# Performance work log

Hardware: AMD Instinct MI355X
Metric: run time of the kernel (lower is better)

The kernel has to match this reference:

```python
import jax, jax.numpy as jnp
import numpy as np

K = 16  # neighbors, incl. self


def setup_inputs() -> dict:
    key = jax.random.key(0)
    ks = jax.random.split(key, 16)
    N, C = 8192, 256  # points, channels (inter_channels == in_channels == C)
    s = 0.05
    inp = {
        'coords': jax.random.uniform(ks[0], (N, 3), dtype=jnp.float32) * 100.0,
        'feats': jax.random.normal(ks[1], (N, C), dtype=jnp.float32),
        'theta_w': jax.random.normal(ks[2], (C, C), dtype=jnp.float32) * s,
        'theta_b': jax.random.normal(ks[3], (C,), dtype=jnp.float32) * s,
        'phi_w': jax.random.normal(ks[4], (C, C), dtype=jnp.float32) * s,
        'phi_b': jax.random.normal(ks[5], (C,), dtype=jnp.float32) * s,
        'g_w': jax.random.normal(ks[6], (C, C), dtype=jnp.float32) * s,
        'g_b': jax.random.normal(ks[7], (C,), dtype=jnp.float32) * s,
        'pe1_w1': jax.random.normal(ks[8], (3, C), dtype=jnp.float32) * s,
        'pe1_b1': jax.random.normal(ks[9], (C,), dtype=jnp.float32) * s,
        'pe1_w2': jax.random.normal(ks[10], (C, C), dtype=jnp.float32) * s,
        'pe1_b2': jax.random.normal(ks[11], (C,), dtype=jnp.float32) * s,
        'W_w': jax.random.normal(ks[12], (C, C), dtype=jnp.float32) * s,
        'W_b': jax.random.normal(ks[13], (C,), dtype=jnp.float32) * s,
    }
    return inp


def reference(coords, feats, theta_w, theta_b, phi_w, phi_b, g_w, g_b,
              pe1_w1, pe1_b1, pe1_w2, pe1_b2, W_w, W_b):
    C = feats.shape[-1]
    # KNN (squared dists, includes self as nearest) == pytorch3d knn_points
    sq = jnp.sum(coords * coords, axis=-1)  # [N]
    d2 = sq[:, None] + sq[None, :] - 2.0 * (coords @ coords.T)  # [N,N]
    _, idx = jax.lax.top_k(-d2, K)  # [N,K] sorted by ascending distance

    nn_coords = coords[idx]            # [N,K,3] knn gather
    nn_feats = feats[idx]              # [N,K,C]

    theta_f = feats @ theta_w + theta_b          # [N,C]
    phi_f = nn_feats @ phi_w + phi_b             # [N,K,C]

    delta_coords = nn_coords - coords[:, None, :]  # [N,K,3]
    # pe1 MLP; NOTE: original code uses pe1 for both pe1 and pe2 (shared)
    pe = jax.nn.relu(delta_coords @ pe1_w1 + pe1_b1) @ pe1_w2 + pe1_b2  # [N,K,C]

    delta_features = (pe * (theta_f[:, None, :] - phi_f) + pe) / jnp.sqrt(jnp.float32(C))
    sim = jax.nn.softmax(delta_features, axis=1)  # softmax over K neighbors

    g_feats = nn_feats @ g_w + g_b               # [N,K,C]
    y = jnp.sum(sim * g_feats, axis=1)           # [N,C]

    # W (1x1 Minkowski conv == per-point linear) + residual
    return y @ W_w + W_b + feats
```

## Files before the change

kernel.cpp:

```cpp
#include <hip/hip_runtime.h>

typedef __bf16 bf16_t;
typedef bf16_t bf16x8 __attribute__((ext_vector_type(8)));
typedef bf16_t bf16x4 __attribute__((ext_vector_type(4)));
typedef bf16_t bf16x2 __attribute__((ext_vector_type(2)));
typedef float f32x4 __attribute__((ext_vector_type(4)));
typedef unsigned long long u64;

#define N_PTS 8192
#define C_DIM 256
#define K_NN 16

#define GRID_G    16
#define GRID_NC   (GRID_G * GRID_G * GRID_G)
#define GRID_CELL 6.25f
#define GRID_INV  0.16f

__global__ __launch_bounds__(256) void cast_feats_kernel(const float* __restrict__ f,
                                                         bf16_t* __restrict__ fb) {
    int i = (blockIdx.x * 256 + threadIdx.x) * 4;
    float4 v = *(const float4*)(f + i);
    bf16x4 o;
    o[0] = (bf16_t)v.x; o[1] = (bf16_t)v.y; o[2] = (bf16_t)v.z; o[3] = (bf16_t)v.w;
    *(bf16x4*)(fb + i) = o;
}

__global__ __launch_bounds__(256) void prep_weights_kernel(
    const float* __restrict__ w0, const float* __restrict__ w1,
    const float* __restrict__ w2, const float* __restrict__ w3,
    const float* __restrict__ w4, bf16_t* __restrict__ wt_base) {
    int m = blockIdx.y;
    const float* src = (m == 0) ? w0 : (m == 1) ? w1 : (m == 2) ? w2 : (m == 3) ? w3 : w4;
    bf16_t* dst = wt_base + m * (C_DIM * C_DIM);
#pragma unroll
    for (int i = 0; i < 4; ++i) {
        int o = blockIdx.x * 1024 + i * 256 + threadIdx.x;
        int tkb = o >> 9;
        int rem = o & 511;
        int lm = rem >> 5;
        int r = rem & 31;
        int k = (tkb & 7) * 32 + r;
        int n = (tkb >> 3) * 16 + lm;
        dst[o] = (bf16_t)src[k * C_DIM + n];
    }
}

__global__ __launch_bounds__(256) void grid_zero_kernel(int* __restrict__ cellCount,
                                                        int* __restrict__ gcount) {
    int i = blockIdx.x * 256 + threadIdx.x;
    cellCount[i] = 0;
    if (i == 0) *gcount = 0;
}

__global__ __launch_bounds__(256) void grid_count_kernel(const float* __restrict__ coords,
                                                         int* __restrict__ cellCount,
                                                         int* __restrict__ cid) {
    int i = blockIdx.x * 256 + threadIdx.x;
    float x = coords[3 * i + 0], y = coords[3 * i + 1], z = coords[3 * i + 2];
    int cx = (int)(x * GRID_INV); if (cx > GRID_G - 1) cx = GRID_G - 1;
    int cy = (int)(y * GRID_INV); if (cy > GRID_G - 1) cy = GRID_G - 1;
    int cz = (int)(z * GRID_INV); if (cz > GRID_G - 1) cz = GRID_G - 1;
    int c = (cx * GRID_G + cy) * GRID_G + cz;
    cid[i] = c;
    atomicAdd(&cellCount[c], 1);
}

__global__ __launch_bounds__(256) void grid_scan_kernel(const int* __restrict__ cellCount,
                                                        int* __restrict__ cellStart,
                                                        int* __restrict__ cellPtr) {
    __shared__ int part[256];
    int t = threadIdx.x;
    int base = t * 16;
    int v[16];
    int sum = 0;
#pragma unroll
    for (int i = 0; i < 16; ++i) { v[i] = cellCount[base + i]; sum += v[i]; }
    part[t] = sum;
    __syncthreads();
    for (int off = 1; off < 256; off <<= 1) {
        int x = (t >= off) ? part[t - off] : 0;
        __syncthreads();
        part[t] += x;
        __syncthreads();
    }
    int acc = part[t] - sum;
#pragma unroll
    for (int i = 0; i < 16; ++i) {
        cellStart[base + i] = acc;
        cellPtr[base + i] = acc;
        acc += v[i];
    }
    if (t == 255) cellStart[GRID_NC] = acc;
}

__global__ __launch_bounds__(256) void grid_scatter_kernel(
    const float* __restrict__ coords, const int* __restrict__ cid, int* __restrict__ cellPtr,
    float* __restrict__ sx, float* __restrict__ sy, float* __restrict__ sz,
    float* __restrict__ ssq, int* __restrict__ sidx) {
    int i = blockIdx.x * 256 + threadIdx.x;
    int c = cid[i];
    int pos = atomicAdd(&cellPtr[c], 1);
    float x = coords[3 * i + 0], y = coords[3 * i + 1], z = coords[3 * i + 2];
    sx[pos] = x; sy[pos] = y; sz[pos] = z;
    ssq[pos] = __fadd_rn(__fadd_rn(__fmul_rn(x, x), __fmul_rn(y, y)), __fmul_rn(z, z));
    sidx[pos] = i;
}

__global__ __launch_bounds__(256) void knn_grid_kernel(
    const float* __restrict__ coords, const int* __restrict__ cellStart,
    const float* __restrict__ sx, const float* __restrict__ sy,
    const float* __restrict__ sz, const float* __restrict__ ssq,
    const int* __restrict__ sidx,
    int* __restrict__ idx_out, int* __restrict__ glist, int* __restrict__ gcount) {
    const int tid = threadIdx.x;
    const int wave = tid >> 6, lane = tid & 63;
    const int q = blockIdx.x * 4 + wave;

    __shared__ int segBase[4][25];
    __shared__ int segPref[4][26];
    __shared__ u64 cand[4][256];
    __shared__ int cnt[4];

    if (lane == 0) cnt[wave] = 0;

    const float qx = coords[3 * q + 0], qy = coords[3 * q + 1], qz = coords[3 * q + 2];
    const float sqi = __fadd_rn(__fadd_rn(__fmul_rn(qx, qx), __fmul_rn(qy, qy)),
                                __fmul_rn(qz, qz));

    int cx = (int)(qx * GRID_INV); if (cx > GRID_G - 1) cx = GRID_G - 1;
    int cy = (int)(qy * GRID_INV); if (cy > GRID_G - 1) cy = GRID_G - 1;
    int cz = (int)(qz * GRID_INV); if (cz > GRID_G - 1) cz = GRID_G - 1;
    int wx0 = cx - 2; if (wx0 < 0) wx0 = 0;
    int wx1 = cx + 2; if (wx1 > GRID_G - 1) wx1 = GRID_G - 1;
    int wy0 = cy - 2; if (wy0 < 0) wy0 = 0;
    int wy1 = cy + 2; if (wy1 > GRID_G - 1) wy1 = GRID_G - 1;
    int wz0 = cz - 2; if (wz0 < 0) wz0 = 0;
    int wz1 = cz + 2; if (wz1 > GRID_G - 1) wz1 = GRID_G - 1;

    const float INF = __int_as_float(0x7f800000);
    float rc = INF;
    if (wx0 > 0)          rc = fminf(rc, qx - (float)wx0 * GRID_CELL);
    if (wx1 < GRID_G - 1) rc = fminf(rc, (float)(wx1 + 1) * GRID_CELL - qx);
    if (wy0 > 0)          rc = fminf(rc, qy - (float)wy0 * GRID_CELL);
    if (wy1 < GRID_G - 1) rc = fminf(rc, (float)(wy1 + 1) * GRID_CELL - qy);
    if (wz0 > 0)          rc = fminf(rc, qz - (float)wz0 * GRID_CELL);
    if (wz1 < GRID_G - 1) rc = fminf(rc, (float)(wz1 + 1) * GRID_CELL - qz);
    float rc2 = rc * rc * 0.9999f;

    int nx = wx1 - wx0 + 1, nyc = wy1 - wy0 + 1;
    int ns = nx * nyc;
    if (lane < ns) {
        int scx = wx0 + lane / nyc;
        int scy = wy0 + lane % nyc;
        int b = (scx * GRID_G + scy) * GRID_G;
        int s0 = cellStart[b + wz0];
        int s1 = cellStart[b + wz1 + 1];
        segBase[wave][lane] = s0;
        segPref[wave][lane] = s1 - s0;
    }
    __syncthreads();
    if (lane == 0) {
        int acc = 0;
        for (int s = 0; s < ns; ++s) { int l = segPref[wave][s]; segPref[wave][s] = acc; acc += l; }
        segPref[wave][ns] = acc;
    }
    __syncthreads();

    const int M = segPref[wave][ns];
    bool flag = (M < K_NN);

    float lmin = INF;
    {
        int s = 0;
        for (int t = lane; t < M; t += 64) {
            while (t >= segPref[wave][s + 1]) ++s;
            int pos = segBase[wave][s] + (t - segPref[wave][s]);
            float x = sx[pos], y = sy[pos], z = sz[pos], sj = ssq[pos];
            float dot = __fmaf_rn(z, qz, __fmaf_rn(y, qy, __fmul_rn(x, qx)));
            float d2 = __fsub_rn(__fadd_rn(sqi, sj), __fmul_rn(2.0f, dot));
            lmin = fminf(lmin, d2);
        }
    }
    float g = fminf(lmin, __shfl_xor(lmin, 1));
    g = fminf(g, __shfl_xor(g, 2));
    float tau = fmaxf(g, __shfl_xor(g, 4));
    tau = fmaxf(tau, __shfl_xor(tau, 8));
    tau = fmaxf(tau, __shfl_xor(tau, 16));
    tau = fmaxf(tau, __shfl_xor(tau, 32));

    {
        int s = 0;
        for (int t = lane; t < M; t += 64) {
            while (t >= segPref[wave][s + 1]) ++s;
            int pos = segBase[wave][s] + (t - segPref[wave][s]);
            float x = sx[pos], y = sy[pos], z = sz[pos], sj = ssq[pos];
            float dot = __fmaf_rn(z, qz, __fmaf_rn(y, qy, __fmul_rn(x, qx)));
            float d2 = __fsub_rn(__fadd_rn(sqi, sj), __fmul_rn(2.0f, dot));
            if (d2 <= tau) {
                unsigned u = __float_as_uint(d2);
                u = (u & 0x80000000u) ? ~u : (u | 0x80000000u);
                int slot = atomicAdd(&cnt[wave], 1);
                if (slot < 256)
                    cand[wave][slot] = (((u64)u) << 32) | (unsigned)sidx[pos];
            }
        }
    }
    __syncthreads();

    int m = cnt[wave];
    if (m > 256) { flag = true; m = 256; }
    u64 k0 = ~0ull, k1 = ~0ull, k2 = ~0ull, k3 = ~0ull;
    if (lane < m) k0 = cand[wave][lane];
    if (lane + 64 < m) k1 = cand[wave][lane + 64];
    if (lane + 128 < m) k2 = cand[wave][lane + 128];
    if (lane + 192 < m) k3 = cand[wave][lane + 192];
    u64 lm2 = k0; int li = 0;
    if (k1 < lm2) { lm2 = k1; li = 1; }
    if (k2 < lm2) { lm2 = k2; li = 2; }
    if (k3 < lm2) { lm2 = k3; li = 3; }
    int keep = 0;
    u64 last = ~0ull;
#pragma unroll 1
    for (int r = 0; r < 16; ++r) {
        u64 w = lm2;
#pragma unroll
        for (int off = 1; off < 64; off <<= 1) {
            u64 o = __shfl_xor(w, off);
            w = (o < w) ? o : w;
        }
        if (lane == r) keep = (int)(unsigned)(w & 0xffffffffull);
        last = w;
        if (lm2 == w) {
            if (li == 0) k0 = ~0ull;
            else if (li == 1) k1 = ~0ull;
            else if (li == 2) k2 = ~0ull;
            else k3 = ~0ull;
            lm2 = k0; li = 0;
            if (k1 < lm2) { lm2 = k1; li = 1; }
            if (k2 < lm2) { lm2 = k2; li = 2; }
            if (k3 < lm2) { lm2 = k3; li = 3; }
        }
    }

    if (!flag) {
        unsigned ou = (unsigned)(last >> 32);
        unsigned db = (ou & 0x80000000u) ? (ou ^ 0x80000000u) : ~ou;
        float d16 = __uint_as_float(db);
        if (d16 >= rc2) flag = true;
    }
    if (flag && lane == 0) {
        int sl = atomicAdd(gcount, 1);
        glist[sl] = q;
    }
    if (lane < 16) idx_out[q * K_NN + lane] = keep;
}

__global__ __launch_bounds__(256) void knn_fallback_kernel(const float* __restrict__ coords,
                                                           const int* __restrict__ glist,
                                                           const int* __restrict__ gcount,
                                                           int* __restrict__ idx_out) {
    const int count = *gcount;
    const int n0 = blockIdx.x * 4;
    if (n0 >= count) return;

    const int tid = threadIdx.x;
    const int wave = tid >> 6, lane = tid & 63;
    __shared__ float red16[4][16];
    __shared__ u64 cand[4][256];
    __shared__ int cnt[4];
    __shared__ int qids[4];

    if (tid < 4) {
        cnt[tid] = 0;
        int slot = n0 + tid;
        qids[tid] = glist[slot < count ? slot : count - 1];
    }
    __syncthreads();

    float qx[4], qy[4], qz[4], sqi[4];
#pragma unroll
    for (int q = 0; q < 4; ++q) {
        int id = qids[q];
        qx[q] = coords[3 * id + 0];
        qy[q] = coords[3 * id + 1];
        qz[q] = coords[3 * id + 2];
        sqi[q] = __fadd_rn(__fadd_rn(__fmul_rn(qx[q], qx[q]), __fmul_rn(qy[q], qy[q])),
                           __fmul_rn(qz[q], qz[q]));
    }

    const float INF = __int_as_float(0x7f800000);
    const float* cp = coords + tid * 96;

    float lmin[4] = {INF, INF, INF, INF};
#pragma unroll
    for (int c = 0; c < 4; ++c) {
        float buf[24];
#pragma unroll
        for (int v = 0; v < 6; ++v)
            *(float4*)(buf + v * 4) = *(const float4*)(cp + c * 24 + v * 4);
#pragma unroll
        for (int p = 0; p < 8; ++p) {
            float x = buf[3 * p + 0], y = buf[3 * p + 1], z = buf[3 * p + 2];
            float sqj = __fadd_rn(__fadd_rn(__fmul_rn(x, x), __fmul_rn(y, y)),
                                  __fmul_rn(z, z));
#pragma unroll
            for (int q = 0; q < 4; ++q) {
                float dot = __fmaf_rn(z, qz[q], __fmaf_rn(y, qy[q], __fmul_rn(x, qx[q])));
                float d2 = __fsub_rn(__fadd_rn(sqi[q], sqj), __fmul_rn(2.0f, dot));
                lmin[q] = fminf(lmin[q], d2);
            }
        }
    }

#pragma unroll
    for (int q = 0; q < 4; ++q) {
        float g = lmin[q];
        g = fminf(g, __shfl_xor(g, 1));
        g = fminf(g, __shfl_xor(g, 2));
        g = fminf(g, __shfl_xor(g, 4));
        g = fminf(g, __shfl_xor(g, 8));
        if ((lane & 15) == 0) red16[q][wave * 4 + (lane >> 4)] = g;
    }
    __syncthreads();

    float tau[4];
#pragma unroll
    for (int q = 0; q < 4; ++q) {
        float t = red16[q][0];
#pragma unroll
        for (int i = 1; i < 16; ++i) t = fmaxf(t, red16[q][i]);
        tau[q] = t;
    }

#pragma unroll
    for (int c = 0; c < 4; ++c) {
        float buf[24];
#pragma unroll
        for (int v = 0; v < 6; ++v)
            *(float4*)(buf + v * 4) = *(const float4*)(cp + c * 24 + v * 4);
#pragma unroll
        for (int p = 0; p < 8; ++p) {
            float x = buf[3 * p + 0], y = buf[3 * p + 1], z = buf[3 * p + 2];
            float sqj = __fadd_rn(__fadd_rn(__fmul_rn(x, x), __fmul_rn(y, y)),
                                  __fmul_rn(z, z));
            int j = tid * 32 + c * 8 + p;
#pragma unroll
            for (int q = 0; q < 4; ++q) {
                float dot = __fmaf_rn(z, qz[q], __fmaf_rn(y, qy[q], __fmul_rn(x, qx[q])));
                float d2 = __fsub_rn(__fadd_rn(sqi[q], sqj), __fmul_rn(2.0f, dot));
                if (d2 <= tau[q]) {
                    unsigned u = __float_as_uint(d2);
                    u = (u & 0x80000000u) ? ~u : (u | 0x80000000u);
                    int slot = atomicAdd(&cnt[q], 1);
                    if (slot < 256)
                        cand[q][slot] = (((u64)u) << 32) | (unsigned)j;
                }
            }
        }
    }
    __syncthreads();

    int m = cnt[wave]; if (m > 256) m = 256;
    u64 k0 = ~0ull, k1 = ~0ull, k2 = ~0ull, k3 = ~0ull;
    if (lane < m) k0 = cand[wave][lane];
    if (lane + 64 < m) k1 = cand[wave][lane + 64];
    if (lane + 128 < m) k2 = cand[wave][lane + 128];
    if (lane + 192 < m) k3 = cand[wave][lane + 192];
    u64 lm2 = k0; int li = 0;
    if (k1 < lm2) { lm2 = k1; li = 1; }
    if (k2 < lm2) { lm2 = k2; li = 2; }
    if (k3 < lm2) { lm2 = k3; li = 3; }
    int keep = 0;
#pragma unroll 1
    for (int r = 0; r < 16; ++r) {
        u64 w = lm2;
#pragma unroll
        for (int off = 1; off < 64; off <<= 1) {
            u64 o = __shfl_xor(w, off);
            w = (o < w) ? o : w;
        }
        if (lane == r) keep = (int)(unsigned)(w & 0xffffffffull);
        if (lm2 == w) {
            if (li == 0) k0 = ~0ull;
            else if (li == 1) k1 = ~0ull;
            else if (li == 2) k2 = ~0ull;
            else k3 = ~0ull;
            lm2 = k0; li = 0;
            if (k1 < lm2) { lm2 = k1; li = 1; }
            if (k2 < lm2) { lm2 = k2; li = 2; }
            if (k3 < lm2) { lm2 = k3; li = 3; }
        }
    }
    if (lane < 16) idx_out[qids[wave] * K_NN + lane] = keep;
}

__global__ __launch_bounds__(256, 2) void proj_kernel(
    const bf16_t* __restrict__ fb, const bf16_t* __restrict__ wt_base,
    const float* __restrict__ tb, const float* __restrict__ pb, const float* __restrict__ gb,
    float* __restrict__ T, bf16_t* __restrict__ PG) {
    const int sel = blockIdx.y;
    const bf16_t* Wt = wt_base + sel * (C_DIM * C_DIM);
    const float* bias = (sel == 0) ? tb : (sel == 1) ? pb : gb;
    const int wave = threadIdx.x >> 6, lane = threadIdx.x & 63;
    const int q = lane >> 4, lm = lane & 15;
    const int m0 = blockIdx.x * 64;

    bf16x8 bfr[4][8];
#pragma unroll
    for (int ti = 0; ti < 4; ++ti)
#pragma unroll
        for (int kb = 0; kb < 8; ++kb)
            bfr[ti][kb] = *(const bf16x8*)(Wt + (((wave * 4 + ti) * 8 + kb) << 9) + lm * 32 + q * 8);

    float bv[4];
#pragma unroll
    for (int ti = 0; ti < 4; ++ti) bv[ti] = bias[(wave * 4 + ti) * 16 + lm];

#pragma unroll
    for (int p = 0; p < 4; ++p) {
        const bf16_t* arow = fb + (m0 + p * 16 + lm) * C_DIM + q * 8;
        bf16x8 a[8];
#pragma unroll
        for (int kb = 0; kb < 8; ++kb) a[kb] = *(const bf16x8*)(arow + kb * 32);
        f32x4 acc[4];
#pragma unroll
        for (int ti = 0; ti < 4; ++ti) acc[ti] = (f32x4){0.f, 0.f, 0.f, 0.f};
#pragma unroll
        for (int ti = 0; ti < 4; ++ti)
#pragma unroll
            for (int kb = 0; kb < 8; ++kb)
                acc[ti] = __builtin_amdgcn_mfma_f32_16x16x32_bf16(a[kb], bfr[ti][kb], acc[ti], 0, 0, 0);

#pragma unroll
        for (int ti = 0; ti < 4; ++ti) {
            int c = (wave * 4 + ti) * 16 + lm;
#pragma unroll
            for (int r = 0; r < 4; ++r) {
                float v = acc[ti][r] + bv[ti];
                int off = (m0 + p * 16 + q * 4 + r) * C_DIM + c;
                if (sel == 0) T[off] = v;
                else if (sel == 1) PG[2 * off] = (bf16_t)v;
                else PG[2 * off + 1] = (bf16_t)v;
            }
        }
    }
}

#define HPAD 264
#define P_BLK 4
#define HROWS (P_BLK * 16)
__global__ __launch_bounds__(256, 2) void pe2_fused_kernel(
    const float* __restrict__ coords, const int* __restrict__ idx,
    const float* __restrict__ T, const bf16_t* __restrict__ PG,
    const float* __restrict__ w1, const float* __restrict__ b1, const float* __restrict__ b2,
    const bf16_t* __restrict__ Wt2, bf16_t* __restrict__ yb) {
    __shared__ __align__(16) bf16_t h_lds[HROWS * HPAD];
    __shared__ float dxyz[HROWS][3];
    __shared__ int idxl[HROWS];
    const int tid = threadIdx.x;
    const int p0 = blockIdx.x * P_BLK;
    const int wave = tid >> 6, lane = tid & 63;
    const int q = lane >> 4, lm = lane & 15;

    bf16x8 bfr[4][8];
#pragma unroll
    for (int ti = 0; ti < 4; ++ti)
#pragma unroll
        for (int kb = 0; kb < 8; ++kb)
            bfr[ti][kb] = *(const bf16x8*)(Wt2 + (((wave * 4 + ti) * 8 + kb) << 9) + lm * 32 + q * 8);
    float b2c[4];
#pragma unroll
    for (int ti = 0; ti < 4; ++ti) b2c[ti] = b2[(wave * 4 + ti) * 16 + lm];

    if (tid < HROWS) {
        int n = p0 + (tid >> 4);
        int j = idx[n * K_NN + (tid & 15)];
        idxl[tid] = j;
        dxyz[tid][0] = coords[3 * j + 0] - coords[3 * n + 0];
        dxyz[tid][1] = coords[3 * j + 1] - coords[3 * n + 1];
        dxyz[tid][2] = coords[3 * j + 2] - coords[3 * n + 2];
    }
    __syncthreads();

    {
        int c = tid;
        float wx = w1[c], wy = w1[C_DIM + c], wz = w1[2 * C_DIM + c], bb = b1[c];
#pragma unroll 4
        for (int r = 0; r < HROWS; ++r) {
            float pre = dxyz[r][0] * wx + dxyz[r][1] * wy + dxyz[r][2] * wz + bb;
            h_lds[r * HPAD + c] = (bf16_t)fmaxf(pre, 0.0f);
        }
    }
    __syncthreads();

#pragma unroll 1
    for (int lp = 0; lp < P_BLK; ++lp) {
        const int n = p0 + lp;

        int jr[4];
#pragma unroll
        for (int r = 0; r < 4; ++r) jr[r] = idxl[lp * 16 + q * 4 + r];
        bf16x2 pg[4][4];
        float Tn[4];
#pragma unroll
        for (int ti = 0; ti < 4; ++ti) {
            int c = (wave * 4 + ti) * 16 + lm;
            Tn[ti] = T[n * C_DIM + c];
#pragma unroll
            for (int r = 0; r < 4; ++r)
                pg[ti][r] = *(const bf16x2*)(PG + 2 * (jr[r] * C_DIM + c));
        }

        const bf16_t* hrow = h_lds + (lp * 16 + lm) * HPAD + q * 8;
        bf16x8 a[8];
#pragma unroll
        for (int kb = 0; kb < 8; ++kb) a[kb] = *(const bf16x8*)(hrow + kb * 32);
        f32x4 acc[4];
#pragma unroll
        for (int ti = 0; ti < 4; ++ti) acc[ti] = (f32x4){0.f, 0.f, 0.f, 0.f};
#pragma unroll
        for (int ti = 0; ti < 4; ++ti)
#pragma unroll
            for (int kb = 0; kb < 8; ++kb)
                acc[ti] = __builtin_amdgcn_mfma_f32_16x16x32_bf16(a[kb], bfr[ti][kb], acc[ti], 0, 0, 0);

#pragma unroll
        for (int ti = 0; ti < 4; ++ti) {
            int c = (wave * 4 + ti) * 16 + lm;
            float df[4];
#pragma unroll
            for (int r = 0; r < 4; ++r) {
                float pe = acc[ti][r] + b2c[ti];
                df[r] = (pe * (Tn[ti] - (float)pg[ti][r][0]) + pe) * 0.0625f;
            }
            float mx = fmaxf(fmaxf(df[0], df[1]), fmaxf(df[2], df[3]));
            mx = fmaxf(mx, __shfl_xor(mx, 16));
            mx = fmaxf(mx, __shfl_xor(mx, 32));
            float e[4], s = 0.f;
#pragma unroll
            for (int r = 0; r < 4; ++r) { e[r] = __expf(df[r] - mx); s += e[r]; }
            s += __shfl_xor(s, 16);
            s += __shfl_xor(s, 32);
            float inv = 1.0f / s;
            float y = 0.f;
#pragma unroll
            for (int r = 0; r < 4; ++r) y += e[r] * inv * (float)pg[ti][r][1];
            y += __shfl_xor(y, 16);
            y += __shfl_xor(y, 32);
            if (q == 0) yb[n * C_DIM + c] = (bf16_t)y;
        }
    }
}

__global__ __launch_bounds__(256, 2) void final_kernel(
    const bf16_t* __restrict__ yb, const bf16_t* __restrict__ Wt,
    const float* __restrict__ Wb, const float* __restrict__ feats,
    float* __restrict__ out) {
    const int wave = threadIdx.x >> 6, lane = threadIdx.x & 63;
    const int q = lane >> 4, lm = lane & 15;
    const int m0 = blockIdx.x * 64;

    bf16x8 bfr[4][8];
#pragma unroll
    for (int ti = 0; ti < 4; ++ti)
#pragma unroll
        for (int kb = 0; kb < 8; ++kb)
            bfr[ti][kb] = *(const bf16x8*)(Wt + (((wave * 4 + ti) * 8 + kb) << 9) + lm * 32 + q * 8);
    float bv[4];
#pragma unroll
    for (int ti = 0; ti < 4; ++ti) bv[ti] = Wb[(wave * 4 + ti) * 16 + lm];

#pragma unroll
    for (int p = 0; p < 4; ++p) {
        const bf16_t* arow = yb + (m0 + p * 16 + lm) * C_DIM + q * 8;
        bf16x8 a[8];
#pragma unroll
        for (int kb = 0; kb < 8; ++kb) a[kb] = *(const bf16x8*)(arow + kb * 32);
        f32x4 acc[4];
#pragma unroll
        for (int ti = 0; ti < 4; ++ti) acc[ti] = (f32x4){0.f, 0.f, 0.f, 0.f};
#pragma unroll
        for (int ti = 0; ti < 4; ++ti)
#pragma unroll
            for (int kb = 0; kb < 8; ++kb)
                acc[ti] = __builtin_amdgcn_mfma_f32_16x16x32_bf16(a[kb], bfr[ti][kb], acc[ti], 0, 0, 0);

#pragma unroll
        for (int ti = 0; ti < 4; ++ti) {
            int c = (wave * 4 + ti) * 16 + lm;
#pragma unroll
            for (int r = 0; r < 4; ++r) {
                int off = (m0 + p * 16 + q * 4 + r) * C_DIM + c;
                out[off] = acc[ti][r] + bv[ti] + feats[off];
            }
        }
    }
}

extern "C" void kernel_launch(void* const* d_in, const int* in_sizes, int n_in,
                              void* d_out, int out_size, void* d_ws, size_t ws_size,
                              hipStream_t stream) {
    const float* coords = (const float*)d_in[0];
    const float* feats  = (const float*)d_in[1];
    const float* theta_w = (const float*)d_in[2];
    const float* theta_b = (const float*)d_in[3];
    const float* phi_w   = (const float*)d_in[4];
    const float* phi_b   = (const float*)d_in[5];
    const float* g_w     = (const float*)d_in[6];
    const float* g_b     = (const float*)d_in[7];
    const float* pe1_w1  = (const float*)d_in[8];
    const float* pe1_b1  = (const float*)d_in[9];
    const float* pe1_w2  = (const float*)d_in[10];
    const float* pe1_b2  = (const float*)d_in[11];
    const float* W_w     = (const float*)d_in[12];
    const float* W_b     = (const float*)d_in[13];
    float* out = (float*)d_out;

    char* w = (char*)d_ws;
    size_t off = 0;
    int* idx = (int*)(w + off);        off += (size_t)N_PTS * K_NN * 4;
    bf16_t* fb = (bf16_t*)(w + off);   off += (size_t)N_PTS * C_DIM * 2;
    bf16_t* wt = (bf16_t*)(w + off);   off += (size_t)5 * C_DIM * C_DIM * 2;
    float* T = (float*)(w + off);      off += (size_t)N_PTS * C_DIM * 4;
    bf16_t* PG = (bf16_t*)(w + off);   off += (size_t)N_PTS * C_DIM * 4;
    bf16_t* yb = (bf16_t*)(w + off);   off += (size_t)N_PTS * C_DIM * 2;
    int* cid       = (int*)(w + off);  off += (size_t)N_PTS * 4;
    int* cellCount = (int*)(w + off);  off += (size_t)GRID_NC * 4;
    int* cellStart = (int*)(w + off);  off += (size_t)(GRID_NC + 1) * 4;
    int* cellPtr   = (int*)(w + off);  off += (size_t)GRID_NC * 4;
    float* sxp = (float*)(w + off);    off += (size_t)N_PTS * 4;
    float* syp = (float*)(w + off);    off += (size_t)N_PTS * 4;
    float* szp = (float*)(w + off);    off += (size_t)N_PTS * 4;
    float* ssqp = (float*)(w + off);   off += (size_t)N_PTS * 4;
    int* sidxp = (int*)(w + off);      off += (size_t)N_PTS * 4;
    int* glist = (int*)(w + off);      off += (size_t)N_PTS * 4;
    int* gcount = (int*)(w + off);     off += 256;
    (void)ws_size; (void)in_sizes; (void)n_in; (void)out_size;

    cast_feats_kernel<<<(N_PTS * C_DIM) / 1024, 256, 0, stream>>>(feats, fb);
    prep_weights_kernel<<<dim3(64, 5), 256, 0, stream>>>(theta_w, phi_w, g_w, pe1_w2, W_w, wt);

    grid_zero_kernel<<<GRID_NC / 256, 256, 0, stream>>>(cellCount, gcount);
    grid_count_kernel<<<N_PTS / 256, 256, 0, stream>>>(coords, cellCount, cid);
    grid_scan_kernel<<<1, 256, 0, stream>>>(cellCount, cellStart, cellPtr);
    grid_scatter_kernel<<<N_PTS / 256, 256, 0, stream>>>(coords, cid, cellPtr,
                                                         sxp, syp, szp, ssqp, sidxp);
    knn_grid_kernel<<<N_PTS / 4, 256, 0, stream>>>(coords, cellStart, sxp, syp, szp,
                                                   ssqp, sidxp, idx, glist, gcount);
    knn_fallback_kernel<<<N_PTS / 4, 256, 0, stream>>>(coords, glist, gcount, idx);

    proj_kernel<<<dim3(N_PTS / 64, 3), 256, 0, stream>>>(fb, wt, theta_b, phi_b, g_b, T, PG);
    pe2_fused_kernel<<<N_PTS / P_BLK, 256, 0, stream>>>(coords, idx, T, PG,
                                                        pe1_w1, pe1_b1, pe1_b2,
                                                        wt + 3 * C_DIM * C_DIM, yb);
    final_kernel<<<N_PTS / 64, 256, 0, stream>>>(yb, wt + 4 * C_DIM * C_DIM, W_b, feats, out);
}
```

Before: 226.0 us.

## Fuse grid build, feature cast and weight prep into one kernel; enlarge pe2 block

Merges six small launches (feature cast, weight transpose/cast, grid zero/count/scan/scatter) into a single kernel. Block 0 builds the whole spatial grid using LDS atomics, while the other blocks do the casts concurrently. This removes launch overhead and the global-memory round trips for cell counts. Separately, pe2_fused_kernel now processes 8 points per block instead of 4. That doubles its LDS tile and may reduce occupancy.

```diff
diff --git a/kernel.cpp b/kernel.cpp
--- a/kernel.cpp
+++ b/kernel.cpp
@@ -16,94 +16,97 @@
 #define GRID_CELL 6.25f
 #define GRID_INV  0.16f
 
-__global__ __launch_bounds__(256) void cast_feats_kernel(const float* __restrict__ f,
-                                                         bf16_t* __restrict__ fb) {
-    int i = (blockIdx.x * 256 + threadIdx.x) * 4;
-    float4 v = *(const float4*)(f + i);
-    bf16x4 o;
-    o[0] = (bf16_t)v.x; o[1] = (bf16_t)v.y; o[2] = (bf16_t)v.z; o[3] = (bf16_t)v.w;
-    *(bf16x4*)(fb + i) = o;
-}
-
-__global__ __launch_bounds__(256) void prep_weights_kernel(
+#define CAST_NBLK 2048
+#define PREPW_NBLK 320
+__global__ __launch_bounds__(256) void fused_prep_kernel(
+    const float* __restrict__ feats, bf16_t* __restrict__ fb,
     const float* __restrict__ w0, const float* __restrict__ w1,
     const float* __restrict__ w2, const float* __restrict__ w3,
-    const float* __restrict__ w4, bf16_t* __restrict__ wt_base) {
-    int m = blockIdx.y;
-    const float* src = (m == 0) ? w0 : (m == 1) ? w1 : (m == 2) ? w2 : (m == 3) ? w3 : w4;
-    bf16_t* dst = wt_base + m * (C_DIM * C_DIM);
-#pragma unroll
-    for (int i = 0; i < 4; ++i) {
-        int o = blockIdx.x * 1024 + i * 256 + threadIdx.x;
-        int tkb = o >> 9;
-        int rem = o & 511;
-        int lm = rem >> 5;
-        int r = rem & 31;
-        int k = (tkb & 7) * 32 + r;
-        int n = (tkb >> 3) * 16 + lm;
-        dst[o] = (bf16_t)src[k * C_DIM + n];
-    }
-}
-
-__global__ __launch_bounds__(256) void grid_zero_kernel(int* __restrict__ cellCount,
-                                                        int* __restrict__ gcount) {
-    int i = blockIdx.x * 256 + threadIdx.x;
-    cellCount[i] = 0;
-    if (i == 0) *gcount = 0;
-}
-
-__global__ __launch_bounds__(256) void grid_count_kernel(const float* __restrict__ coords,
-                                                         int* __restrict__ cellCount,
-                                                         int* __restrict__ cid) {
-    int i = blockIdx.x * 256 + threadIdx.x;
-    float x = coords[3 * i + 0], y = coords[3 * i + 1], z = coords[3 * i + 2];
-    int cx = (int)(x * GRID_INV); if (cx > GRID_G - 1) cx = GRID_G - 1;
-    int cy = (int)(y * GRID_INV); if (cy > GRID_G - 1) cy = GRID_G - 1;
-    int cz = (int)(z * GRID_INV); if (cz > GRID_G - 1) cz = GRID_G - 1;
-    int c = (cx * GRID_G + cy) * GRID_G + cz;
-    cid[i] = c;
-    atomicAdd(&cellCount[c], 1);
-}
-
-__global__ __launch_bounds__(256) void grid_scan_kernel(const int* __restrict__ cellCount,
-                                                        int* __restrict__ cellStart,
-                                                        int* __restrict__ cellPtr) {
-    __shared__ int part[256];
-    int t = threadIdx.x;
-    int base = t * 16;
-    int v[16];
-    int sum = 0;
-#pragma unroll
-    for (int i = 0; i < 16; ++i) { v[i] = cellCount[base + i]; sum += v[i]; }
-    part[t] = sum;
-    __syncthreads();
-    for (int off = 1; off < 256; off <<= 1) {
-        int x = (t >= off) ? part[t - off] : 0;
+    const float* __restrict__ w4, bf16_t* __restrict__ wt_base,
+    const float* __restrict__ coords, int* __restrict__ cellStart,
+    float* __restrict__ sx, float* __restrict__ sy, float* __restrict__ sz,
+    float* __restrict__ ssq, int* __restrict__ sidx, int* __restrict__ gcount) {
+    const int b = blockIdx.x;
+    const int t = threadIdx.x;
+
+    if (b == 0) {
+        __shared__ int cCnt[GRID_NC];
+        __shared__ int part[256];
+        for (int i = t; i < GRID_NC; i += 256) cCnt[i] = 0;
+        if (t == 0) *gcount = 0;
         __syncthreads();
-        part[t] += x;
+
+        int ci[32];
+#pragma unroll
+        for (int k = 0; k < 32; ++k) {
+            int i = t + k * 256;
+            float x = coords[3 * i + 0], y = coords[3 * i + 1], z = coords[3 * i + 2];
+            int cx = (int)(x * GRID_INV); if (cx > GRID_G - 1) cx = GRID_G - 1;
+            int cy = (int)(y * GRID_INV); if (cy > GRID_G - 1) cy = GRID_G - 1;
+            int cz = (int)(z * GRID_INV); if (cz > GRID_G - 1) cz = GRID_G - 1;
+            int c = (cx * GRID_G + cy) * GRID_G + cz;
+            ci[k] = c;
+            atomicAdd(&cCnt[c], 1);
+        }
         __syncthreads();
-    }
-    int acc = part[t] - sum;
-#pragma unroll
-    for (int i = 0; i < 16; ++i) {
-        cellStart[base + i] = acc;
-        cellPtr[base + i] = acc;
-        acc += v[i];
-    }
-    if (t == 255) cellStart[GRID_NC] = acc;
-}
-
-__global__ __launch_bounds__(256) void grid_scatter_kernel(
-    const float* __restrict__ coords, const int* __restrict__ cid, int* __restrict__ cellPtr,
-    float* __restrict__ sx, float* __restrict__ sy, float* __restrict__ sz,
-    float* __restrict__ ssq, int* __restrict__ sidx) {
-    int i = blockIdx.x * 256 + threadIdx.x;
-    int c = cid[i];
-    int pos = atomicAdd(&cellPtr[c], 1);
-    float x = coords[3 * i + 0], y = coords[3 * i + 1], z = coords[3 * i + 2];
-    sx[pos] = x; sy[pos] = y; sz[pos] = z;
-    ssq[pos] = __fadd_rn(__fadd_rn(__fmul_rn(x, x), __fmul_rn(y, y)), __fmul_rn(z, z));
-    sidx[pos] = i;
+
+        int base = t * 16;
+        int v[16];
+        int sum = 0;
+#pragma unroll
+        for (int i = 0; i < 16; ++i) { v[i] = cCnt[base + i]; sum += v[i]; }
+        part[t] = sum;
+        __syncthreads();
+        for (int off = 1; off < 256; off <<= 1) {
+            int x = (t >= off) ? part[t - off] : 0;
+            __syncthreads();
+            part[t] += x;
+            __syncthreads();
+        }
+        int acc = part[t] - sum;
+#pragma unroll
+        for (int i = 0; i < 16; ++i) {
+            cellStart[base + i] = acc;
+            cCnt[base + i] = acc;
+            acc += v[i];
+        }
+        if (t == 255) cellStart[GRID_NC] = acc;
+        __syncthreads();
+
+#pragma unroll
+        for (int k = 0; k < 32; ++k) {
+            int i = t + k * 256;
+            int c = ci[k];
+            int pos = atomicAdd(&cCnt[c], 1);
+            float x = coords[3 * i + 0], y = coords[3 * i + 1], z = coords[3 * i + 2];
+            sx[pos] = x; sy[pos] = y; sz[pos] = z;
+            ssq[pos] = __fadd_rn(__fadd_rn(__fmul_rn(x, x), __fmul_rn(y, y)), __fmul_rn(z, z));
+            sidx[pos] = i;
+        }
+    } else if (b <= CAST_NBLK) {
+        int i = ((b - 1) * 256 + t) * 4;
+        float4 v = *(const float4*)(feats + i);
+        bf16x4 o;
+        o[0] = (bf16_t)v.x; o[1] = (bf16_t)v.y; o[2] = (bf16_t)v.z; o[3] = (bf16_t)v.w;
+        *(bf16x4*)(fb + i) = o;
+    } else {
+        int pb = b - 1 - CAST_NBLK;
+        int m = pb >> 6;
+        int bx = pb & 63;
+        const float* src = (m == 0) ? w0 : (m == 1) ? w1 : (m == 2) ? w2 : (m == 3) ? w3 : w4;
+        bf16_t* dst = wt_base + m * (C_DIM * C_DIM);
+#pragma unroll
+        for (int i = 0; i < 4; ++i) {
+            int o = bx * 1024 + i * 256 + t;
+            int tkb = o >> 9;
+            int rem = o & 511;
+            int lm = rem >> 5;
+            int r = rem & 31;
+            int k = (tkb & 7) * 32 + r;
+            int n = (tkb >> 3) * 16 + lm;
+            dst[o] = (bf16_t)src[k * C_DIM + n];
+        }
+    }
 }
 
 __global__ __launch_bounds__(256) void knn_grid_kernel(
@@ -447,7 +450,7 @@
 }
 
 #define HPAD 264
-#define P_BLK 4
+#define P_BLK 8
 #define HROWS (P_BLK * 16)
 __global__ __launch_bounds__(256, 2) void pe2_fused_kernel(
     const float* __restrict__ coords, const int* __restrict__ idx,
@@ -624,10 +627,7 @@
     float* T = (float*)(w + off);      off += (size_t)N_PTS * C_DIM * 4;
     bf16_t* PG = (bf16_t*)(w + off);   off += (size_t)N_PTS * C_DIM * 4;
     bf16_t* yb = (bf16_t*)(w + off);   off += (size_t)N_PTS * C_DIM * 2;
-    int* cid       = (int*)(w + off);  off += (size_t)N_PTS * 4;
-    int* cellCount = (int*)(w + off);  off += (size_t)GRID_NC * 4;
     int* cellStart = (int*)(w + off);  off += (size_t)(GRID_NC + 1) * 4;
-    int* cellPtr   = (int*)(w + off);  off += (size_t)GRID_NC * 4;
     float* sxp = (float*)(w + off);    off += (size_t)N_PTS * 4;
     float* syp = (float*)(w + off);    off += (size_t)N_PTS * 4;
     float* szp = (float*)(w + off);    off += (size_t)N_PTS * 4;
@@ -637,14 +637,10 @@
     int* gcount = (int*)(w + off);     off += 256;
     (void)ws_size; (void)in_sizes; (void)n_in; (void)out_size;
 
-    cast_feats_kernel<<<(N_PTS * C_DIM) / 1024, 256, 0, stream>>>(feats, fb);
-    prep_weights_kernel<<<dim3(64, 5), 256, 0, stream>>>(theta_w, phi_w, g_w, pe1_w2, W_w, wt);
-
-    grid_zero_kernel<<<GRID_NC / 256, 256, 0, stream>>>(cellCount, gcount);
-    grid_count_kernel<<<N_PTS / 256, 256, 0, stream>>>(coords, cellCount, cid);
-    grid_scan_kernel<<<1, 256, 0, stream>>>(cellCount, cellStart, cellPtr);
-    grid_scatter_kernel<<<N_PTS / 256, 256, 0, stream>>>(coords, cid, cellPtr,
-                                                         sxp, syp, szp, ssqp, sidxp);
+    fused_prep_kernel<<<1 + CAST_NBLK + PREPW_NBLK, 256, 0, stream>>>(
+        feats, fb, theta_w, phi_w, g_w, pe1_w2, W_w, wt,
+        coords, cellStart, sxp, syp, szp, ssqp, sidxp, gcount);
+
     knn_grid_kernel<<<N_PTS / 4, 256, 0, stream>>>(coords, cellStart, sxp, syp, szp,
                                                    ssqp, sidxp, idx, glist, gcount);
     knn_fallback_kernel<<<N_PTS / 4, 256, 0, stream>>>(coords, glist, gcount, idx);
```

Result: slower. 232.7 us (+3.0%).

## Fuse output projection into pe2 kernel and merge prep kernels

Applied to the files above, without the earlier changes.

Merges the feature cast, weight prep and grid-zero kernels into one launch. It also folds the final W projection plus residual into the pe2 fused kernel, which now stages y in LDS, so the bf16 y round trip through global memory and one launch go away. P_BLK doubles to 8 so each block fills half of a 16-row MFMA tile. The rows above 8 are zero padding, which wastes half the final MFMA work. The larger LDS footprint and reloaded weight fragments may reduce occupancy.

```diff
diff --git a/kernel.cpp b/kernel.cpp
--- a/kernel.cpp
+++ b/kernel.cpp
@@ -16,40 +16,45 @@
 #define GRID_CELL 6.25f
 #define GRID_INV  0.16f
 
-__global__ __launch_bounds__(256) void cast_feats_kernel(const float* __restrict__ f,
-                                                         bf16_t* __restrict__ fb) {
-    int i = (blockIdx.x * 256 + threadIdx.x) * 4;
-    float4 v = *(const float4*)(f + i);
-    bf16x4 o;
-    o[0] = (bf16_t)v.x; o[1] = (bf16_t)v.y; o[2] = (bf16_t)v.z; o[3] = (bf16_t)v.w;
-    *(bf16x4*)(fb + i) = o;
-}
-
-__global__ __launch_bounds__(256) void prep_weights_kernel(
+#define CAST_NBLK 2048
+#define PREPW_NBLK 320
+__global__ __launch_bounds__(256) void prep_kernel(
+    const float* __restrict__ feats, bf16_t* __restrict__ fb,
     const float* __restrict__ w0, const float* __restrict__ w1,
     const float* __restrict__ w2, const float* __restrict__ w3,
-    const float* __restrict__ w4, bf16_t* __restrict__ wt_base) {
-    int m = blockIdx.y;
-    const float* src = (m == 0) ? w0 : (m == 1) ? w1 : (m == 2) ? w2 : (m == 3) ? w3 : w4;
-    bf16_t* dst = wt_base + m * (C_DIM * C_DIM);
-#pragma unroll
-    for (int i = 0; i < 4; ++i) {
-        int o = blockIdx.x * 1024 + i * 256 + threadIdx.x;
-        int tkb = o >> 9;
-        int rem = o & 511;
-        int lm = rem >> 5;
-        int r = rem & 31;
-        int k = (tkb & 7) * 32 + r;
-        int n = (tkb >> 3) * 16 + lm;
-        dst[o] = (bf16_t)src[k * C_DIM + n];
-    }
-}
-
-__global__ __launch_bounds__(256) void grid_zero_kernel(int* __restrict__ cellCount,
-                                                        int* __restrict__ gcount) {
-    int i = blockIdx.x * 256 + threadIdx.x;
-    cellCount[i] = 0;
-    if (i == 0) *gcount = 0;
+    const float* __restrict__ w4, bf16_t* __restrict__ wt_base,
+    int* __restrict__ cellCount, int* __restrict__ gcount) {
+    const int b = blockIdx.x;
+    const int t = threadIdx.x;
+
+    if (b < CAST_NBLK) {
+        int i = (b * 256 + t) * 4;
+        float4 v = *(const float4*)(feats + i);
+        bf16x4 o;
+        o[0] = (bf16_t)v.x; o[1] = (bf16_t)v.y; o[2] = (bf16_t)v.z; o[3] = (bf16_t)v.w;
+        *(bf16x4*)(fb + i) = o;
+    } else if (b < CAST_NBLK + PREPW_NBLK) {
+        int pb = b - CAST_NBLK;
+        int m = pb >> 6;
+        int bx = pb & 63;
+        const float* src = (m == 0) ? w0 : (m == 1) ? w1 : (m == 2) ? w2 : (m == 3) ? w3 : w4;
+        bf16_t* dst = wt_base + m * (C_DIM * C_DIM);
+#pragma unroll
+        for (int i = 0; i < 4; ++i) {
+            int o = bx * 1024 + i * 256 + t;
+            int tkb = o >> 9;
+            int rem = o & 511;
+            int lm = rem >> 5;
+            int r = rem & 31;
+            int k = (tkb & 7) * 32 + r;
+            int n = (tkb >> 3) * 16 + lm;
+            dst[o] = (bf16_t)src[k * C_DIM + n];
+        }
+    } else {
+        int zb = b - CAST_NBLK - PREPW_NBLK;
+        cellCount[zb * 256 + t] = 0;
+        if (zb == 0 && t == 0) *gcount = 0;
+    }
 }
 
 __global__ __launch_bounds__(256) void grid_count_kernel(const float* __restrict__ coords,
@@ -447,14 +452,17 @@
 }
 
 #define HPAD 264
-#define P_BLK 4
+#define P_BLK 8
 #define HROWS (P_BLK * 16)
 __global__ __launch_bounds__(256, 2) void pe2_fused_kernel(
     const float* __restrict__ coords, const int* __restrict__ idx,
     const float* __restrict__ T, const bf16_t* __restrict__ PG,
     const float* __restrict__ w1, const float* __restrict__ b1, const float* __restrict__ b2,
-    const bf16_t* __restrict__ Wt2, bf16_t* __restrict__ yb) {
+    const bf16_t* __restrict__ Wt2, const bf16_t* __restrict__ Wt3,
+    const float* __restrict__ Wb, const float* __restrict__ feats,
+    float* __restrict__ out) {
     __shared__ __align__(16) bf16_t h_lds[HROWS * HPAD];
+    __shared__ __align__(16) bf16_t yl[16][HPAD];
     __shared__ float dxyz[HROWS][3];
     __shared__ int idxl[HROWS];
     const int tid = threadIdx.x;
@@ -471,6 +479,12 @@
     float b2c[4];
 #pragma unroll
     for (int ti = 0; ti < 4; ++ti) b2c[ti] = b2[(wave * 4 + ti) * 16 + lm];
+
+    {
+        bf16x8 z8 = (bf16x8){(bf16_t)0.f, (bf16_t)0.f, (bf16_t)0.f, (bf16_t)0.f,
+                             (bf16_t)0.f, (bf16_t)0.f, (bf16_t)0.f, (bf16_t)0.f};
+        *(bf16x8*)(&yl[8 + (tid >> 5)][(tid & 31) * 8]) = z8;
+    }
 
     if (tid < HROWS) {
         int n = p0 + (tid >> 4);
@@ -547,51 +561,41 @@
             for (int r = 0; r < 4; ++r) y += e[r] * inv * (float)pg[ti][r][1];
             y += __shfl_xor(y, 16);
             y += __shfl_xor(y, 32);
-            if (q == 0) yb[n * C_DIM + c] = (bf16_t)y;
-        }
-    }
-}
-
-__global__ __launch_bounds__(256, 2) void final_kernel(
-    const bf16_t* __restrict__ yb, const bf16_t* __restrict__ Wt,
-    const float* __restrict__ Wb, const float* __restrict__ feats,
-    float* __restrict__ out) {
-    const int wave = threadIdx.x >> 6, lane = threadIdx.x & 63;
-    const int q = lane >> 4, lm = lane & 15;
-    const int m0 = blockIdx.x * 64;
-
-    bf16x8 bfr[4][8];
+            if (q == 0) yl[lp][c] = (bf16_t)y;
+        }
+    }
+    __syncthreads();
+
 #pragma unroll
     for (int ti = 0; ti < 4; ++ti)
 #pragma unroll
         for (int kb = 0; kb < 8; ++kb)
-            bfr[ti][kb] = *(const bf16x8*)(Wt + (((wave * 4 + ti) * 8 + kb) << 9) + lm * 32 + q * 8);
-    float bv[4];
-#pragma unroll
-    for (int ti = 0; ti < 4; ++ti) bv[ti] = Wb[(wave * 4 + ti) * 16 + lm];
-
-#pragma unroll
-    for (int p = 0; p < 4; ++p) {
-        const bf16_t* arow = yb + (m0 + p * 16 + lm) * C_DIM + q * 8;
-        bf16x8 a[8];
-#pragma unroll
-        for (int kb = 0; kb < 8; ++kb) a[kb] = *(const bf16x8*)(arow + kb * 32);
-        f32x4 acc[4];
-#pragma unroll
-        for (int ti = 0; ti < 4; ++ti) acc[ti] = (f32x4){0.f, 0.f, 0.f, 0.f};
-#pragma unroll
-        for (int ti = 0; ti < 4; ++ti)
-#pragma unroll
-            for (int kb = 0; kb < 8; ++kb)
-                acc[ti] = __builtin_amdgcn_mfma_f32_16x16x32_bf16(a[kb], bfr[ti][kb], acc[ti], 0, 0, 0);
-
-#pragma unroll
-        for (int ti = 0; ti < 4; ++ti) {
-            int c = (wave * 4 + ti) * 16 + lm;
-#pragma unroll
-            for (int r = 0; r < 4; ++r) {
-                int off = (m0 + p * 16 + q * 4 + r) * C_DIM + c;
-                out[off] = acc[ti][r] + bv[ti] + feats[off];
+            bfr[ti][kb] = *(const bf16x8*)(Wt3 + (((wave * 4 + ti) * 8 + kb) << 9) + lm * 32 + q * 8);
+    float bw[4];
+#pragma unroll
+    for (int ti = 0; ti < 4; ++ti) bw[ti] = Wb[(wave * 4 + ti) * 16 + lm];
+
+    bf16x8 a2[8];
+#pragma unroll
+    for (int kb = 0; kb < 8; ++kb) a2[kb] = *(const bf16x8*)(&yl[lm][kb * 32 + q * 8]);
+    f32x4 acc2[4];
+#pragma unroll
+    for (int ti = 0; ti < 4; ++ti) acc2[ti] = (f32x4){0.f, 0.f, 0.f, 0.f};
+#pragma unroll
+    for (int ti = 0; ti < 4; ++ti)
+#pragma unroll
+        for (int kb = 0; kb < 8; ++kb)
+            acc2[ti] = __builtin_amdgcn_mfma_f32_16x16x32_bf16(a2[kb], bfr[ti][kb], acc2[ti], 0, 0, 0);
+
+#pragma unroll
+    for (int ti = 0; ti < 4; ++ti) {
+        int c = (wave * 4 + ti) * 16 + lm;
+#pragma unroll
+        for (int r = 0; r < 4; ++r) {
+            int row = q * 4 + r;
+            if (row < P_BLK) {
+                int off = (p0 + row) * C_DIM + c;
+                out[off] = acc2[ti][r] + bw[ti] + feats[off];
             }
         }
     }
@@ -623,7 +627,6 @@
     bf16_t* wt = (bf16_t*)(w + off);   off += (size_t)5 * C_DIM * C_DIM * 2;
     float* T = (float*)(w + off);      off += (size_t)N_PTS * C_DIM * 4;
     bf16_t* PG = (bf16_t*)(w + off);   off += (size_t)N_PTS * C_DIM * 4;
-    bf16_t* yb = (bf16_t*)(w + off);   off += (size_t)N_PTS * C_DIM * 2;
     int* cid       = (int*)(w + off);  off += (size_t)N_PTS * 4;
     int* cellCount = (int*)(w + off);  off += (size_t)GRID_NC * 4;
     int* cellStart = (int*)(w + off);  off += (size_t)(GRID_NC + 1) * 4;
@@ -637,10 +640,9 @@
     int* gcount = (int*)(w + off);     off += 256;
     (void)ws_size; (void)in_sizes; (void)n_in; (void)out_size;
 
-    cast_feats_kernel<<<(N_PTS * C_DIM) / 1024, 256, 0, stream>>>(feats, fb);
-    prep_weights_kernel<<<dim3(64, 5), 256, 0, stream>>>(theta_w, phi_w, g_w, pe1_w2, W_w, wt);
-
-    grid_zero_kernel<<<GRID_NC / 256, 256, 0, stream>>>(cellCount, gcount);
+    prep_kernel<<<CAST_NBLK + PREPW_NBLK + 16, 256, 0, stream>>>(
+        feats, fb, theta_w, phi_w, g_w, pe1_w2, W_w, wt, cellCount, gcount);
+
     grid_count_kernel<<<N_PTS / 256, 256, 0, stream>>>(coords, cellCount, cid);
     grid_scan_kernel<<<1, 256, 0, stream>>>(cellCount, cellStart, cellPtr);
     grid_scatter_kernel<<<N_PTS / 256, 256, 0, stream>>>(coords, cid, cellPtr,
@@ -652,6 +654,7 @@
     proj_kernel<<<dim3(N_PTS / 64, 3), 256, 0, stream>>>(fb, wt, theta_b, phi_b, g_b, T, PG);
     pe2_fused_kernel<<<N_PTS / P_BLK, 256, 0, stream>>>(coords, idx, T, PG,
                                                         pe1_w1, pe1_b1, pe1_b2,
-                                                        wt + 3 * C_DIM * C_DIM, yb);
-    final_kernel<<<N_PTS / 64, 256, 0, stream>>>(yb, wt + 4 * C_DIM * C_DIM, W_b, feats, out);
-}
+                                                        wt + 3 * C_DIM * C_DIM,
+                                                        wt + 4 * C_DIM * C_DIM,
+                                                        W_b, feats, out);
+}
```

New measurement: 214.8 us. 1.05x faster.
